# Performance work log

Hardware: AMD Instinct MI355X
Metric: run time of the kernel (lower is better)

## Reference

```python
import jax, jax.numpy as jnp
import numpy as np

N1 = 8000   # solute nodes
N2 = 8000   # solvent nodes
E = 128000  # edges per graph side (avg degree 16)
B = 128     # number of graphs in the batch
NFEAT, NHID, NCLS = 128, 256, 512
D = 2 * NCLS   # Set2Set input dim (1024)
H = D          # LSTM hidden = input_dim in DGL Set2Set


def setup_inputs() -> dict:
    key = jax.random.key(0)
    ks = jax.random.split(key, 24)
    w = lambda k, shp, fan: (jax.random.normal(k, shp, jnp.float32) / np.sqrt(fan))
    inp = {}
    inp["x1"] = jax.random.normal(ks[0], (N1, NFEAT), jnp.float32)
    inp["x2"] = jax.random.normal(ks[1], (N2, NFEAT), jnp.float32)
    inp["src1"] = jax.random.randint(ks[2], (E,), 0, N1, jnp.int32)
    inp["dst1"] = jax.random.randint(ks[3], (E,), 0, N1, jnp.int32)
    inp["src2"] = jax.random.randint(ks[4], (E,), 0, N2, jnp.int32)
    inp["dst2"] = jax.random.randint(ks[5], (E,), 0, N2, jnp.int32)
    inp["gid1"] = jnp.sort(jax.random.randint(ks[6], (N1,), 0, B, jnp.int32))
    inp["gid2"] = jnp.sort(jax.random.randint(ks[7], (N2,), 0, B, jnp.int32))
    # GraphConv weights (DGL stores W as [in, out]) + biases
    inp["W_gc1"] = w(ks[8], (NFEAT, NHID), NFEAT); inp["b_gc1"] = jnp.zeros((NHID,), jnp.float32)
    inp["W_gc2"] = w(ks[9], (NHID, NCLS), NHID);   inp["b_gc2"] = jnp.zeros((NCLS,), jnp.float32)
    inp["W_gc3"] = w(ks[10], (NFEAT, NHID), NFEAT); inp["b_gc3"] = jnp.zeros((NHID,), jnp.float32)
    inp["W_gc4"] = w(ks[11], (NHID, NCLS), NHID);   inp["b_gc4"] = jnp.zeros((NCLS,), jnp.float32)
    # Set2Set LSTM (input = 2*D, hidden = H), torch gate order i,f,g,o
    inp["W_ih"] = w(ks[12], (4 * H, 2 * D), 2 * D)
    inp["W_hh"] = w(ks[13], (4 * H, H), H)
    inp["b_ih"] = jnp.zeros((4 * H,), jnp.float32)
    inp["b_hh"] = jnp.zeros((4 * H,), jnp.float32)
    # MLP head
    inp["W_fc1"] = w(ks[14], (1024, 4096), 4096); inp["b_fc1"] = jnp.zeros((1024,), jnp.float32)
    inp["W_fc2"] = w(ks[15], (512, 1024), 1024);  inp["b_fc2"] = jnp.zeros((512,), jnp.float32)
    inp["W_fc3"] = w(ks[16], (1, 512), 512);      inp["b_fc3"] = jnp.zeros((1,), jnp.float32)
    return inp


def _gconv(x, src, dst, W, b, n):
    # DGL GraphConv, norm='both': D_out^{-1/2} scaling at src, sum over in-edges, D_in^{-1/2} at dst
    ones = jnp.ones(src.shape[0], x.dtype)
    outd = jnp.clip(jax.ops.segment_sum(ones, src, num_segments=n), 1.0)
    ind = jnp.clip(jax.ops.segment_sum(ones, dst, num_segments=n), 1.0)
    h = (x * (outd ** -0.5)[:, None]) @ W
    agg = jax.ops.segment_sum(h[src], dst, num_segments=n)   # sparse neighbor aggregation
    return agg * (ind ** -0.5)[:, None] + b


def _set2set(x, gid, Wih, Whh, bih, bhh):
    # DGL Set2Set, n_iters=2, 1-layer LSTM; x: [N, D], gid: [N] graph membership
    d = x.shape[1]
    q_star = jnp.zeros((B, 2 * d), x.dtype)
    h = jnp.zeros((B, d), x.dtype)
    c = jnp.zeros((B, d), x.dtype)
    for _ in range(2):
        gates = q_star @ Wih.T + h @ Whh.T + bih + bhh
        i, f, g, o = jnp.split(gates, 4, axis=1)
        c = jax.nn.sigmoid(f) * c + jax.nn.sigmoid(i) * jnp.tanh(g)
        h = jax.nn.sigmoid(o) * jnp.tanh(c)
        e = jnp.sum(x * h[gid], axis=1)                       # per-node attention logit
        m = jax.ops.segment_max(e, gid, num_segments=B)
        ex = jnp.exp(e - m[gid])
        s = jax.ops.segment_sum(ex, gid, num_segments=B)
        alpha = ex / s[gid]                                   # segment softmax
        r = jax.ops.segment_sum(alpha[:, None] * x, gid, num_segments=B)
        q_star = jnp.concatenate([h, r], axis=1)
    return q_star


def reference(x1, x2, src1, dst1, src2, dst2, gid1, gid2,
              W_gc1, b_gc1, W_gc2, b_gc2, W_gc3, b_gc3, W_gc4, b_gc4,
              W_ih, W_hh, b_ih, b_hh,
              W_fc1, b_fc1, W_fc2, b_fc2, W_fc3, b_fc3):
    s = jax.nn.relu(_gconv(x1, src1, dst1, W_gc1, b_gc1, N1))
    s = _gconv(s, src1, dst1, W_gc2, b_gc2, N1)
    v = jax.nn.relu(_gconv(x2, src2, dst2, W_gc3, b_gc3, N2))
    v = _gconv(v, src2, dst2, W_gc4, b_gc4, N2)
    # len_map = len1.T @ len2 == same-graph indicator for binary membership matrices
    len_map = (gid1[:, None] == gid2[None, :]).astype(s.dtype)
    imap = jnp.tanh(s @ v.T) * len_map                        # [N1, N2]
    solvent_prime = imap.T @ s                                # [N2, NCLS]
    solute_prime = imap @ v                                   # [N1, NCLS]
    sf = jnp.concatenate([s, solute_prime], axis=1)           # [N1, 2*NCLS]
    vf = jnp.concatenate([v, solvent_prime], axis=1)
    ss = _set2set(sf, gid1, W_ih, W_hh, b_ih, b_hh)           # [B, 4*NCLS]
    vs = _set2set(vf, gid2, W_ih, W_hh, b_ih, b_hh)
    z = jnp.concatenate([ss, vs], axis=1)                     # [B, 4096]
    z = jax.nn.relu(z @ W_fc1.T + b_fc1)
    z = jax.nn.relu(z @ W_fc2.T + b_fc2)
    return z @ W_fc3.T + b_fc3                                # [B, 1]
```

## Files before the change

kernel.cpp:

```cpp
#include <hip/hip_runtime.h>

#define DEV __device__ __forceinline__

typedef _Float16 half8 __attribute__((ext_vector_type(8)));
typedef _Float16 half4_t __attribute__((ext_vector_type(4)));
typedef float f32x4 __attribute__((ext_vector_type(4)));

DEV float ftanh(float x){
  float ax = fabsf(x);
  float e = __expf(-2.f*ax);
  float t = (1.f - e)/(1.f + e);
  return x < 0.f ? -t : t;
}
DEV float fsigm(float x){ return 1.f/(1.f + expf(-x)); }
DEV float wredsum(float v){
  #pragma unroll
  for (int o=32;o;o>>=1) v += __shfl_xor(v,o,64);
  return v;
}

__global__ void k_zero_i32(int* __restrict__ p, int n){
  int i = blockIdx.x*256 + threadIdx.x; if (i<n) p[i]=0;
}

__global__ void k_hist2(const int* __restrict__ s1, const int* __restrict__ d1, int E1,
                        int* __restrict__ co1, int* __restrict__ ci1,
                        const int* __restrict__ s2, const int* __restrict__ d2, int E2,
                        int* __restrict__ co2, int* __restrict__ ci2){
  int e = blockIdx.x*256 + threadIdx.x;
  if (e < E1){ atomicAdd(&co1[s1[e]],1); atomicAdd(&ci1[d1[e]],1); }
  int f = e - E1;
  if (f >= 0 && f < E2){ atomicAdd(&co2[s2[f]],1); atomicAdd(&ci2[d2[f]],1); }
}

__global__ void k_scan2(const int* __restrict__ c1, int n1, int* __restrict__ r1,
                        const int* __restrict__ c2, int n2, int* __restrict__ r2){
  __shared__ int sm[1024];
  const int* cnt = blockIdx.x ? c2 : c1;
  int*       row = blockIdx.x ? r2 : r1;
  int n          = blockIdx.x ? n2 : n1;
  int t = threadIdx.x;
  int per = n/1024 + 1;
  int st = t*per;
  int s = 0;
  for (int i=st;i<st+per;++i) if (i<n) s += cnt[i];
  sm[t]=s; __syncthreads();
  for (int o=1;o<1024;o<<=1){
    int v = (t>=o)? sm[t-o]:0;
    __syncthreads();
    sm[t] += v;
    __syncthreads();
  }
  int base = sm[t]-s;
  for (int i=st;i<st+per;++i){
    if (i<=n) row[i]=base;
    if (i<n) base += cnt[i];
  }
}

__global__ void k_scale2(const int* __restrict__ co1, const int* __restrict__ ci1, int n1,
                         float* __restrict__ os1, float* __restrict__ is1,
                         const int* __restrict__ co2, const int* __restrict__ ci2, int n2,
                         float* __restrict__ os2, float* __restrict__ is2){
  int i = blockIdx.x*256+threadIdx.x;
  if (i<n1){
    int a = co1[i] > 1 ? co1[i] : 1;
    int b = ci1[i] > 1 ? ci1[i] : 1;
    os1[i] = 1.f/sqrtf((float)a);
    is1[i] = 1.f/sqrtf((float)b);
  }
  int j = i - n1;
  if (j>=0 && j<n2){
    int a = co2[j] > 1 ? co2[j] : 1;
    int b = ci2[j] > 1 ? ci2[j] : 1;
    os2[j] = 1.f/sqrtf((float)a);
    is2[j] = 1.f/sqrtf((float)b);
  }
}

__global__ void k_scatter2(const int* __restrict__ s1, const int* __restrict__ d1, int E1,
                           const int* __restrict__ row1, int* __restrict__ cur1, int* __restrict__ csr1,
                           const int* __restrict__ s2, const int* __restrict__ d2, int E2,
                           const int* __restrict__ row2, int* __restrict__ cur2, int* __restrict__ csr2){
  int e = blockIdx.x*256+threadIdx.x;
  if (e<E1){ int d=d1[e]; int p=atomicAdd(&cur1[d],1); csr1[row1[d]+p]=s1[e]; }
  int f = e - E1;
  if (f>=0 && f<E2){ int d=d2[f]; int p=atomicAdd(&cur2[d],1); csr2[row2[d]+p]=s2[f]; }
}

__global__ void k_goff2(const int* __restrict__ g1, int n1, int* __restrict__ o1,
                        const int* __restrict__ g2, int n2, int* __restrict__ o2, int B){
  int t = threadIdx.x;
  const int* gid = (t>=256)? g2 : g1;
  int*      goff = (t>=256)? o2 : o1;
  int n          = (t>=256)? n2 : n1;
  int q = t & 255;
  if (q<=B){
    int lo=0, hi=n;
    while (lo<hi){ int mid=(lo+hi)>>1; if (gid[mid]<q) lo=mid+1; else hi=mid; }
    goff[q]=lo;
  }
}

__global__ void k_agg_h(const float* __restrict__ x, int ldx, const float* __restrict__ osc,
                        const int* __restrict__ row, const int* __restrict__ csr,
                        _Float16* __restrict__ oh, _Float16* __restrict__ ol, int n, int f4shift){
  int F4 = 1<<f4shift;
  int node = blockIdx.x*(256>>f4shift) + (threadIdx.x>>f4shift);
  if (node>=n) return;
  int fc = threadIdx.x & (F4-1);
  int F = F4<<2;
  int rs=row[node], re=row[node+1];
  float ax=0, ay=0, az=0, aw=0;
  if (osc){
    for (int e=rs;e<re;++e){
      int s = csr[e];
      float sc = osc[s];
      const float4 v = *(const float4*)(x + (size_t)s*ldx + (fc<<2));
      ax += sc*v.x; ay += sc*v.y; az += sc*v.z; aw += sc*v.w;
    }
  } else {
    int e = rs;
    for (; e+1<re; e+=2){
      int s0 = csr[e], s1 = csr[e+1];
      const float4 v0 = *(const float4*)(x + (size_t)s0*ldx + (fc<<2));
      const float4 v1 = *(const float4*)(x + (size_t)s1*ldx + (fc<<2));
      ax += v0.x+v1.x; ay += v0.y+v1.y; az += v0.z+v1.z; aw += v0.w+v1.w;
    }
    if (e<re){
      int s0 = csr[e];
      const float4 v0 = *(const float4*)(x + (size_t)s0*ldx + (fc<<2));
      ax += v0.x; ay += v0.y; az += v0.z; aw += v0.w;
    }
  }
  half4_t hv, lv;
  hv.x = (_Float16)ax; lv.x = (_Float16)(ax - (float)hv.x);
  hv.y = (_Float16)ay; lv.y = (_Float16)(ay - (float)hv.y);
  hv.z = (_Float16)az; lv.z = (_Float16)(az - (float)hv.z);
  hv.w = (_Float16)aw; lv.w = (_Float16)(aw - (float)hv.w);
  size_t o = (size_t)node*F + (fc<<2);
  *(half4_t*)(oh + o) = hv;
  *(half4_t*)(ol + o) = lv;
}

__global__ void k_wpack4(const float* __restrict__ W0, const float* __restrict__ W1,
                         const float* __restrict__ W2, const float* __restrict__ W3,
                         _Float16* __restrict__ h0, _Float16* __restrict__ l0,
                         _Float16* __restrict__ h1, _Float16* __restrict__ l1,
                         _Float16* __restrict__ h2, _Float16* __restrict__ l2,
                         _Float16* __restrict__ h3, _Float16* __restrict__ l3){
  int w = blockIdx.y;
  const float* W = (w==0)?W0:(w==1)?W1:(w==2)?W2:W3;
  _Float16* oh = (w==0)?h0:(w==1)?h1:(w==2)?h2:h3;
  _Float16* ol = (w==0)?l0:(w==1)?l1:(w==2)?l2:l3;
  int K   = (w&1)? 256 : 128;
  int nsh = (w&1)? 9 : 8;
  int i = blockIdx.x*256 + threadIdx.x;
  if (i >= (K<<nsh)) return;
  int k = i >> nsh, n = i & ((1<<nsh)-1);
  float v = W[i];
  _Float16 h = (_Float16)v;
  _Float16 l = (_Float16)(v - (float)h);
  size_t p = (((size_t)(k>>3)<<nsh) + n)*8 + (k&7);
  oh[p] = h; ol[p] = l;
}

__global__ __launch_bounds__(256)
void k_gconv_mfma(const _Float16* __restrict__ Ah0, const _Float16* __restrict__ Al0,
                  const _Float16* __restrict__ Ah1, const _Float16* __restrict__ Al1,
                  const _Float16* __restrict__ Bh0, const _Float16* __restrict__ Bl0,
                  const _Float16* __restrict__ Bh1, const _Float16* __restrict__ Bl1,
                  float* __restrict__ C0, float* __restrict__ C1, int ldc,
                  int M0, int M1, int N, int K,
                  const float* __restrict__ rs0, const float* __restrict__ rs1,
                  const float* __restrict__ bi0, const float* __restrict__ bi1, int relu,
                  const float* __restrict__ po0, const float* __restrict__ po1)
{
  __shared__ __align__(16) _Float16 As[2][4096];
  __shared__ __align__(16) _Float16 Bs[2][4096];

  const int gx = gridDim.x, gxy = gridDim.x*gridDim.y;
  const int nwg = gxy*2;
  int fid = blockIdx.x + gx*blockIdx.y + gxy*blockIdx.z;
  int q = nwg>>3, r = nwg&7;
  int xcd = fid & 7, idx = fid >> 3;
  int sid = (xcd<r ? xcd*(q+1) : r*(q+1)+(xcd-r)*q) + idx;
  const int z  = sid / gxy;  int rem = sid - z*gxy;
  const int by = rem / gx,  bx = rem - by*gx;

  const _Float16* Ah = z ? Ah1 : Ah0;
  const _Float16* Al = z ? Al1 : Al0;
  const _Float16* Bh = z ? Bh1 : Bh0;
  const _Float16* Bl = z ? Bl1 : Bl0;
  float*       C  = z ? C1 : C0;
  const float* rsc = z ? rs1 : rs0;
  const float* bia = z ? bi1 : bi0;
  const float* po  = z ? po1 : po0;
  const int M = z ? M1 : M0;

  const int row0 = by << 7;
  const int col0 = bx << 7;
  if (row0 >= ((M+127)&~127)) return;

  const int tid = threadIdx.x;
  const int am  = tid >> 2;
  const int akb = tid & 3;
  const int bn  = tid & 127;
  const int bkb = tid >> 7;
  const int wid = tid >> 6, lane = tid & 63;
  const int wr = wid >> 1, wc = wid & 1;
  const int lr = lane & 15, lg = lane >> 4;

  const size_t ldb8 = (size_t)N * 8;
  f32x4 acc[4][4] = {};

  const int kpt = K >> 5;
  const int nt  = 3 * kpt;

  half8 ga0, ga1, gb0, gb1;
  {
    const _Float16* Ap = Ah + (size_t)(row0 + am) * K + (akb<<3);
    ga0 = *(const half8*)(Ap);
    ga1 = *(const half8*)(Ap + (size_t)64 * K);
    const _Float16* Bp = Bh + (size_t)bkb * ldb8 + (size_t)(col0 + bn) * 8;
    gb0 = *(const half8*)(Bp);
    gb1 = *(const half8*)(Bp + 2*ldb8);
  }
  *(half8*)&As[0][(akb*128 + am)*8]        = ga0;
  *(half8*)&As[0][(akb*128 + am + 64)*8]   = ga1;
  *(half8*)&Bs[0][(bkb*128 + bn)*8]        = gb0;
  *(half8*)&Bs[0][((bkb+2)*128 + bn)*8]    = gb1;
  __syncthreads();

  int term = 0, kk = 32;
  if (kk == K){ kk = 0; term = 1; }
  for (int t = 0; t < nt; ++t){
    const int cb = t & 1;
    if (t + 1 < nt){
      const _Float16* Asrc = (term == 1) ? Al : Ah;
      const _Float16* Bsrc = (term == 2) ? Bl : Bh;
      const _Float16* Ap = Asrc + (size_t)(row0 + am) * K + kk + (akb<<3);
      ga0 = *(const half8*)(Ap);
      ga1 = *(const half8*)(Ap + (size_t)64 * K);
      const _Float16* Bp = Bsrc + (size_t)((kk>>3) + bkb) * ldb8 + (size_t)(col0 + bn) * 8;
      gb0 = *(const half8*)(Bp);
      gb1 = *(const half8*)(Bp + 2*ldb8);
      kk += 32; if (kk == K){ kk = 0; ++term; }
    }
    {
      const _Float16* Abase = &As[cb][((lg<<7) + (wr<<6) + lr)<<3];
      const _Float16* Bbase = &Bs[cb][((lg<<7) + (wc<<6) + lr)<<3];
      half8 af[4], bf[4];
      #pragma unroll
      for (int i=0;i<4;++i){
        af[i] = *(const half8*)(Abase + i*128);
        bf[i] = *(const half8*)(Bbase + i*128);
      }
      #pragma unroll
      for (int mi=0; mi<4; ++mi){
        #pragma unroll
        for (int ni=0; ni<4; ++ni){
          acc[mi][ni] = __builtin_amdgcn_mfma_f32_16x16x32_f16(af[mi], bf[ni], acc[mi][ni], 0, 0, 0);
        }
      }
    }
    if (t + 1 < nt){
      const int nb = cb ^ 1;
      *(half8*)&As[nb][(akb*128 + am)*8]      = ga0;
      *(half8*)&As[nb][(akb*128 + am + 64)*8] = ga1;
      *(half8*)&Bs[nb][(bkb*128 + bn)*8]      = gb0;
      *(half8*)&Bs[nb][((bkb+2)*128 + bn)*8]  = gb1;
    }
    __syncthreads();
  }

  #pragma unroll
  for (int ni = 0; ni < 4; ++ni){
    int cc = col0 + (wc<<6) + (ni<<4) + lr;
    float bv = bia ? bia[cc] : 0.f;
    #pragma unroll
    for (int mi = 0; mi < 4; ++mi){
      int rbase = row0 + (wr<<6) + (mi<<4) + (lg<<2);
      #pragma unroll
      for (int j = 0; j < 4; ++j){
        int rr = rbase + j;
        if (rr < M){
          float rs_ = rsc ? rsc[rr] : 1.f;
          float v = acc[mi][ni][j]*rs_ + bv;
          if (relu) v = fmaxf(v, 0.f);
          if (po) v *= po[rr];
          C[(size_t)rr*ldc + cc] = v;
        }
      }
    }
  }
}

__global__ __launch_bounds__(256)
void k_gemmsk(const float* __restrict__ Ab, size_t AsideOff, int lda,
              const float* __restrict__ Bm, int ldb,
              float* __restrict__ P, int M, int N, int kchunk)
{
  __shared__ float As[2][16][132];
  __shared__ float Bs[2][16][68];
  const int tid = threadIdx.x;
  const int col0 = (int)blockIdx.x << 6;
  const int kbeg = (int)blockIdx.z * kchunk;
  const float* A = Ab + (size_t)blockIdx.y * AsideOff;
  const int ar = tid >> 1, ak = (tid & 1) << 3;
  const int br = tid >> 2, bk = (tid & 3) << 2;
  const int tx = tid & 15, ty = tid >> 4;
  const float* Arow = A + (size_t)ar * lda + kbeg + ak;
  const float* Brow = Bm + (size_t)(col0 + br) * ldb + kbeg + bk;
  float acc[8][4] = {};
  float4 a0 = *(const float4*)(Arow);
  float4 a1 = *(const float4*)(Arow + 4);
  float4 b0 = *(const float4*)(Brow);
  As[0][ak+0][ar]=a0.x; As[0][ak+1][ar]=a0.y; As[0][ak+2][ar]=a0.z; As[0][ak+3][ar]=a0.w;
  As[0][ak+4][ar]=a1.x; As[0][ak+5][ar]=a1.y; As[0][ak+6][ar]=a1.z; As[0][ak+7][ar]=a1.w;
  Bs[0][bk+0][br]=b0.x; Bs[0][bk+1][br]=b0.y; Bs[0][bk+2][br]=b0.z; Bs[0][bk+3][br]=b0.w;
  __syncthreads();
  const int nt = kchunk >> 4;
  for (int t = 0; t < nt; ++t){
    const int cb = t & 1;
    if (t + 1 < nt){
      int k0 = (t + 1) << 4;
      a0 = *(const float4*)(Arow + k0);
      a1 = *(const float4*)(Arow + k0 + 4);
      b0 = *(const float4*)(Brow + k0);
    }
    #pragma unroll
    for (int kk = 0; kk < 16; ++kk){
      float4 b4 = *(const float4*)&Bs[cb][kk][tx << 2];
      float4 a4 = *(const float4*)&As[cb][kk][ty << 3];
      float4 a5 = *(const float4*)&As[cb][kk][(ty << 3) + 4];
      acc[0][0]+=a4.x*b4.x; acc[0][1]+=a4.x*b4.y; acc[0][2]+=a4.x*b4.z; acc[0][3]+=a4.x*b4.w;
      acc[1][0]+=a4.y*b4.x; acc[1][1]+=a4.y*b4.y; acc[1][2]+=a4.y*b4.z; acc[1][3]+=a4.y*b4.w;
      acc[2][0]+=a4.z*b4.x; acc[2][1]+=a4.z*b4.y; acc[2][2]+=a4.z*b4.z; acc[2][3]+=a4.z*b4.w;
      acc[3][0]+=a4.w*b4.x; acc[3][1]+=a4.w*b4.y; acc[3][2]+=a4.w*b4.z; acc[3][3]+=a4.w*b4.w;
      acc[4][0]+=a5.x*b4.x; acc[4][1]+=a5.x*b4.y; acc[4][2]+=a5.x*b4.z; acc[4][3]+=a5.x*b4.w;
      acc[5][0]+=a5.y*b4.x; acc[5][1]+=a5.y*b4.y; acc[5][2]+=a5.y*b4.z; acc[5][3]+=a5.y*b4.w;
      acc[6][0]+=a5.z*b4.x; acc[6][1]+=a5.z*b4.y; acc[6][2]+=a5.z*b4.z; acc[6][3]+=a5.z*b4.w;
      acc[7][0]+=a5.w*b4.x; acc[7][1]+=a5.w*b4.y; acc[7][2]+=a5.w*b4.z; acc[7][3]+=a5.w*b4.w;
    }
    if (t + 1 < nt){
      const int nb = cb ^ 1;
      As[nb][ak+0][ar]=a0.x; As[nb][ak+1][ar]=a0.y; As[nb][ak+2][ar]=a0.z; As[nb][ak+3][ar]=a0.w;
      As[nb][ak+4][ar]=a1.x; As[nb][ak+5][ar]=a1.y; As[nb][ak+6][ar]=a1.z; As[nb][ak+7][ar]=a1.w;
      Bs[nb][bk+0][br]=b0.x; Bs[nb][bk+1][br]=b0.y; Bs[nb][bk+2][br]=b0.z; Bs[nb][bk+3][br]=b0.w;
    }
    __syncthreads();
  }
  float* Pz = P + (size_t)(blockIdx.y*gridDim.z + blockIdx.z) * M * N;
  #pragma unroll
  for (int i = 0; i < 8; ++i){
    int rr = (ty << 3) + i;
    float4 v = {acc[i][0], acc[i][1], acc[i][2], acc[i][3]};
    *(float4*)(Pz + (size_t)rr*N + col0 + (tx<<2)) = v;
  }
}

__global__ void k_red_bias(const float* __restrict__ P, int split, int MN, int N,
                           const float* __restrict__ bias, float* __restrict__ C, int relu){
  int i = blockIdx.x*256 + threadIdx.x;
  if (i >= MN) return;
  float v = bias[i & (N-1)];
  for (int s=0;s<split;++s) v += P[(size_t)s*MN + i];
  if (relu) v = fmaxf(v, 0.f);
  C[i] = v;
}

__global__ __launch_bounds__(256)
void k_pairdot(const float* __restrict__ sf, const float* __restrict__ vf,
               const int* __restrict__ go1, const int* __restrict__ go2, float* __restrict__ T)
{
  __shared__ float As[16][68];
  __shared__ float Bs[16][68];
  int g = blockIdx.z;
  int it = blockIdx.y, jt = blockIdx.x;
  int gox = go1[g]; int cx = go1[g+1]-gox; if (cx>128) cx=128;
  int goy = go2[g]; int cy = go2[g+1]-goy; if (cy>128) cy=128;
  int cx64=(cx+63)&~63, cy64=(cy+63)&~63;
  int i0 = it<<6, j0 = jt<<6;
  if (i0 >= cx64 || j0 >= cy64) return;
  int tid=threadIdx.x, tx=tid&15, ty=tid>>4;
  int a_r = tid>>2, a_k=(tid&3)<<2;
  const float* Arow = sf + (size_t)(gox+i0+a_r)*1024;
  const float* Brow = vf + (size_t)(goy+j0+a_r)*1024;
  bool act = ((i0+(ty<<2)) < cx) && ((j0+(tx<<2)) < cy);
  float acc[4][4]={};
  for (int k0=0;k0<512;k0+=16){
    float4 av = *(const float4*)(Arow + k0 + a_k);
    float4 bv = *(const float4*)(Brow + k0 + a_k);
    As[a_k+0][a_r]=av.x; As[a_k+1][a_r]=av.y; As[a_k+2][a_r]=av.z; As[a_k+3][a_r]=av.w;
    Bs[a_k+0][a_r]=bv.x; Bs[a_k+1][a_r]=bv.y; Bs[a_k+2][a_r]=bv.z; Bs[a_k+3][a_r]=bv.w;
    __syncthreads();
    if (act){
      float4 a4 = *(const float4*)&As[0][ty<<2];
      float4 b4 = *(const float4*)&Bs[0][tx<<2];
      #pragma unroll
      for (int kk=0;kk<16;++kk){
        float4 na, nb;
        if (kk<15){
          na = *(const float4*)&As[kk+1][ty<<2];
          nb = *(const float4*)&Bs[kk+1][tx<<2];
        }
        acc[0][0] += a4.x*b4.x; acc[0][1] += a4.x*b4.y; acc[0][2] += a4.x*b4.z; acc[0][3] += a4.x*b4.w;
        acc[1][0] += a4.y*b4.x; acc[1][1] += a4.y*b4.y; acc[1][2] += a4.y*b4.z; acc[1][3] += a4.y*b4.w;
        acc[2][0] += a4.z*b4.x; acc[2][1] += a4.z*b4.y; acc[2][2] += a4.z*b4.z; acc[2][3] += a4.z*b4.w;
        acc[3][0] += a4.w*b4.x; acc[3][1] += a4.w*b4.y; acc[3][2] += a4.w*b4.z; acc[3][3] += a4.w*b4.w;
        if (kk<15){ a4 = na; b4 = nb; }
      }
    }
    __syncthreads();
  }
  float* Tg = T + (size_t)g*16384;
  #pragma unroll
  for (int ii=0; ii<4; ++ii){
    int gi = i0 + (ty<<2) + ii;
    int gj = j0 + (tx<<2);
    float4 v;
    v.x = (gi<cx && gj+0<cy) ? ftanh(acc[ii][0]) : 0.f;
    v.y = (gi<cx && gj+1<cy) ? ftanh(acc[ii][1]) : 0.f;
    v.z = (gi<cx && gj+2<cy) ? ftanh(acc[ii][2]) : 0.f;
    v.w = (gi<cx && gj+3<cy) ? ftanh(acc[ii][3]) : 0.f;
    *(float4*)(Tg + (size_t)gi*128 + gj) = v;
  }
}

template<bool TRANS>
__global__ __launch_bounds__(256)
void k_outapply(const float* __restrict__ T, const float* __restrict__ other,
                float* __restrict__ own, const int* __restrict__ goOwn, const int* __restrict__ goOther)
{
  __shared__ float As[16][68];
  __shared__ float Bs[16][68];
  int g = blockIdx.z;
  int r0 = (int)blockIdx.y<<6;
  int f0 = (int)blockIdx.x<<6;
  int gown = goOwn[g];   int cown = goOwn[g+1]-gown;   if (cown>128) cown=128;
  int goth = goOther[g]; int coth = goOther[g+1]-goth; if (coth>128) coth=128;
  int cr64 = (cown+63)&~63;
  if (r0 >= cr64) return;
  int K16 = (coth+15)&~15;
  const float* Tg = T + (size_t)g*16384;
  int tid=threadIdx.x, tx=tid&15, ty=tid>>4;
  bool act = (r0 + (ty<<2)) < cown;
  float acc[4][4]={};
  for (int ks=0; ks<K16; ks+=16){
    if (!TRANS){
      int rr = tid>>2, k4 = (tid&3)<<2;
      float4 av = *(const float4*)(Tg + (size_t)(r0+rr)*128 + ks + k4);
      As[k4+0][rr]=av.x; As[k4+1][rr]=av.y; As[k4+2][rr]=av.z; As[k4+3][rr]=av.w;
    } else {
      int kk = tid>>4, r4 = (tid&15)<<2;
      *(float4*)&As[kk][r4] = *(const float4*)(Tg + (size_t)(ks+kk)*128 + r0 + r4);
    }
    int bk = tid>>4, bf = (tid&15)<<2;
    *(float4*)&Bs[bk][bf] = *(const float4*)(other + (size_t)(goth+ks+bk)*1024 + f0 + bf);
    __syncthreads();
    if (act){
      float4 a4 = *(const float4*)&As[0][ty<<2];
      float4 b4 = *(const float4*)&Bs[0][tx<<2];
      #pragma unroll
      for (int kk=0;kk<16;++kk){
        float4 na, nb;
        if (kk<15){
          na = *(const float4*)&As[kk+1][ty<<2];
          nb = *(const float4*)&Bs[kk+1][tx<<2];
        }
        acc[0][0] += a4.x*b4.x; acc[0][1] += a4.x*b4.y; acc[0][2] += a4.x*b4.z; acc[0][3] += a4.x*b4.w;
        acc[1][0] += a4.y*b4.x; acc[1][1] += a4.y*b4.y; acc[1][2] += a4.y*b4.z; acc[1][3] += a4.y*b4.w;
        acc[2][0] += a4.z*b4.x; acc[2][1] += a4.z*b4.y; acc[2][2] += a4.z*b4.z; acc[2][3] += a4.z*b4.w;
        acc[3][0] += a4.w*b4.x; acc[3][1] += a4.w*b4.y; acc[3][2] += a4.w*b4.z; acc[3][3] += a4.w*b4.w;
        if (kk<15){ a4 = na; b4 = nb; }
      }
    }
    __syncthreads();
  }
  #pragma unroll
  for (int ii=0; ii<4; ++ii){
    int rr = r0 + (ty<<2) + ii;
    if (rr < cown){
      float4 v = {acc[ii][0],acc[ii][1],acc[ii][2],acc[ii][3]};
      *(float4*)(own + (size_t)(gown+rr)*1024 + 512 + f0 + (tx<<2)) = v;
    }
  }
}

__global__ void k_lstm1(const float* __restrict__ bih, const float* __restrict__ bhh,
                        float* __restrict__ c1, float* __restrict__ h1){
  int j = blockIdx.x*256 + threadIdx.x;
  if (j >= 1024) return;
  float gi = bih[j]        + bhh[j];
  float gg = bih[j+2048]   + bhh[j+2048];
  float go = bih[j+3072]   + bhh[j+3072];
  float cc = fsigm(gi)*ftanh(gg);
  c1[j] = cc;
  h1[j] = fsigm(go)*ftanh(cc);
}

__global__ void k_gemv_u(const float* __restrict__ Wih, const float* __restrict__ Whh,
                         const float* __restrict__ bih, const float* __restrict__ bhh,
                         const float* __restrict__ h1, float* __restrict__ u){
  int w = (blockIdx.x*256 + threadIdx.x)>>6;
  int lane = threadIdx.x & 63;
  if (w >= 4096) return;
  const float* wi = Wih + (size_t)w*2048;
  const float* wh = Whh + (size_t)w*1024;
  float acc = 0.f;
  #pragma unroll
  for (int qq=0;qq<4;++qq){
    int o = qq*256 + (lane<<2);
    float4 hv = *(const float4*)(h1 + o);
    float4 a  = *(const float4*)(wi + o);
    float4 b  = *(const float4*)(wh + o);
    acc += hv.x*(a.x+b.x) + hv.y*(a.y+b.y) + hv.z*(a.z+b.z) + hv.w*(a.w+b.w);
  }
  acc = wredsum(acc);
  if (lane==0) u[w] = acc + bih[w] + bhh[w];
}

__global__ __launch_bounds__(256)
void k_attn(const float* __restrict__ sf, const float* __restrict__ vf,
            const int* __restrict__ go1, const int* __restrict__ go2,
            const float* __restrict__ hbase, size_t hSideOff, int hstride,
            float* __restrict__ outbase, size_t oSideOff, int ldout)
{
  __shared__ float hs[1024];
  __shared__ float ech[1024];
  __shared__ float red[8];
  int side = blockIdx.y;
  const float* x = side? vf : sf;
  const int* goff = side? go2 : go1;
  const float* hsrc = hbase + (size_t)side*hSideOff;
  float* outp = outbase + (size_t)side*oSideOff;
  int b = blockIdx.x, t = threadIdx.x;
  int i0 = goff[b], i1 = goff[b+1];
  int lane = t & 63, wv = t >> 6;
  { float4 hv = *(const float4*)(hsrc + (size_t)b*hstride + (t<<2));
    *(float4*)&hs[t<<2] = hv; }
  __syncthreads();
  float m = -3.0e38f, s = 0.f;
  float ax=0, ay=0, az=0, aw=0;
  for (int c = i0; c < i1; c += 1024){
    int ce = c + 1024; if (ce > i1) ce = i1;
    int n = ce - c;
    float wmax = -3.0e38f;
    for (int i = c + wv; i < ce; i += 4){
      const float* xr = x + (size_t)i*1024;
      float d = 0.f;
      #pragma unroll
      for (int qq=0;qq<4;++qq){
        int o = qq*256 + (lane<<2);
        float4 xv = *(const float4*)(xr+o);
        float4 h4 = *(const float4*)&hs[o];
        d += xv.x*h4.x + xv.y*h4.y + xv.z*h4.z + xv.w*h4.w;
      }
      d = wredsum(d);
      if (lane==0) ech[i-c] = d;
      wmax = fmaxf(wmax, d);
    }
    if (lane==0) red[wv] = wmax;
    __syncthreads();
    float cm = fmaxf(fmaxf(red[0],red[1]), fmaxf(red[2],red[3]));
    float nm = fmaxf(m, cm);
    float scale = __expf(m - nm);
    s *= scale; ax*=scale; ay*=scale; az*=scale; aw*=scale;
    float ps = 0.f;
    for (int k = t; k < n; k += 256) ps += __expf(ech[k]-nm);
    ps = wredsum(ps);
    __syncthreads();
    if (lane==0) red[wv] = ps;
    __syncthreads();
    s += red[0]+red[1]+red[2]+red[3];
    for (int k = 0; k < n; ++k){
      float w = __expf(ech[k]-nm);
      float4 xv = *(const float4*)(x + (size_t)(c+k)*1024 + (t<<2));
      ax += w*xv.x; ay += w*xv.y; az += w*xv.z; aw += w*xv.w;
    }
    m = nm;
    __syncthreads();
  }
  float inv = (i1>i0 && s>0.f) ? 1.f/s : 0.f;
  float4 o = {ax*inv, ay*inv, az*inv, aw*inv};
  *(float4*)(outp + (size_t)b*ldout + (t<<2)) = o;
}

__global__ void k_lstm2_red(const float* __restrict__ Pb, size_t PsideOff, int split,
                            const float* __restrict__ u, const float* __restrict__ c1,
                            float* __restrict__ z, int B){
  int idx = blockIdx.x*256 + threadIdx.x;
  if (idx >= B*1024) return;
  int side = blockIdx.y;
  const float* P = Pb + (size_t)side*PsideOff;
  int b = idx >> 10, j = idx & 1023;
  float gi=u[j], gf=u[j+1024], gg=u[j+2048], go=u[j+3072];
  const float* g = P + (size_t)b*4096;
  for (int s=0;s<split;++s){
    const float* gs = g + (size_t)s*B*4096;
    gi += gs[j]; gf += gs[j+1024]; gg += gs[j+2048]; go += gs[j+3072];
  }
  float cc = fsigm(gf)*c1[j] + fsigm(gi)*ftanh(gg);
  z[(size_t)b*4096 + side*2048 + j] = fsigm(go)*ftanh(cc);
}

__global__ void k_fc3(const float* __restrict__ z2, const float* __restrict__ w3,
                      const float* __restrict__ b3, float* __restrict__ out, int B){
  int wv = (blockIdx.x*256+threadIdx.x)>>6;
  int lane = threadIdx.x & 63;
  if (wv >= B) return;
  const float* zr = z2 + (size_t)wv*512;
  float acc=0.f;
  #pragma unroll
  for (int qq=0;qq<2;++qq){
    int o = qq*256 + (lane<<2);
    float4 a  = *(const float4*)(zr + o);
    float4 ww = *(const float4*)(w3 + o);
    acc += a.x*ww.x + a.y*ww.y + a.z*ww.z + a.w*ww.w;
  }
  acc = wredsum(acc);
  if (lane==0) out[wv] = acc + b3[0];
}

extern "C" void kernel_launch(void* const* d_in, const int* in_sizes, int n_in,
                              void* d_out, int out_size, void* d_ws, size_t ws_size,
                              hipStream_t stream)
{
  const float* x1  = (const float*)d_in[0];
  const float* x2  = (const float*)d_in[1];
  const int* src1  = (const int*)d_in[2];
  const int* dst1  = (const int*)d_in[3];
  const int* src2  = (const int*)d_in[4];
  const int* dst2  = (const int*)d_in[5];
  const int* gid1  = (const int*)d_in[6];
  const int* gid2  = (const int*)d_in[7];
  const float* Wg1 = (const float*)d_in[8];  const float* bg1 = (const float*)d_in[9];
  const float* Wg2 = (const float*)d_in[10]; const float* bg2 = (const float*)d_in[11];
  const float* Wg3 = (const float*)d_in[12]; const float* bg3 = (const float*)d_in[13];
  const float* Wg4 = (const float*)d_in[14]; const float* bg4 = (const float*)d_in[15];
  const float* Wih = (const float*)d_in[16]; const float* Whh = (const float*)d_in[17];
  const float* bih = (const float*)d_in[18]; const float* bhh = (const float*)d_in[19];
  const float* Wf1 = (const float*)d_in[20]; const float* bf1 = (const float*)d_in[21];
  const float* Wf2 = (const float*)d_in[22]; const float* bf2 = (const float*)d_in[23];
  const float* Wf3 = (const float*)d_in[24]; const float* bf3 = (const float*)d_in[25];
  float* out = (float*)d_out;

  const int N1 = in_sizes[0]/128;
  const int N2 = in_sizes[1]/128;
  const int E1 = in_sizes[2];
  const int E2 = in_sizes[4];
  const int B  = out_size;
  const int NM = N1>N2?N1:N2;

  char* base = (char*)d_ws; size_t off=0;
  auto alloc = [&](size_t bytes)->void*{ void* p = base+off; off += (bytes+255)&~(size_t)255; return p; };

  int* zr   = (int*)alloc(sizeof(int)*(size_t)(3*N1+3*N2));
  int* co1=zr, *ci1=zr+N1, *cur1=zr+2*N1;
  int* co2=zr+3*N1, *ci2=zr+3*N1+N2, *cur2=zr+3*N1+2*N2;
  int* row1 = (int*)alloc(sizeof(int)*(size_t)(N1+1));
  int* row2 = (int*)alloc(sizeof(int)*(size_t)(N2+1));
  int* csr1 = (int*)alloc(sizeof(int)*(size_t)E1);
  int* csr2 = (int*)alloc(sizeof(int)*(size_t)E2);
  int* go1  = (int*)alloc(sizeof(int)*(size_t)(B+1));
  int* go2  = (int*)alloc(sizeof(int)*(size_t)(B+1));
  float* os1 = (float*)alloc(sizeof(float)*(size_t)N1);
  float* is1 = (float*)alloc(sizeof(float)*(size_t)N1);
  float* os2 = (float*)alloc(sizeof(float)*(size_t)N2);
  float* is2 = (float*)alloc(sizeof(float)*(size_t)N2);
  _Float16* a1h = (_Float16*)alloc(sizeof(_Float16)*(size_t)(NM+128)*256);
  _Float16* a1l = (_Float16*)alloc(sizeof(_Float16)*(size_t)(NM+128)*256);
  _Float16* a2h = (_Float16*)alloc(sizeof(_Float16)*(size_t)(NM+128)*256);
  _Float16* a2l = (_Float16*)alloc(sizeof(_Float16)*(size_t)(NM+128)*256);
  _Float16* wg1h = (_Float16*)alloc(sizeof(_Float16)*32768);
  _Float16* wg1l = (_Float16*)alloc(sizeof(_Float16)*32768);
  _Float16* wg2h = (_Float16*)alloc(sizeof(_Float16)*131072);
  _Float16* wg2l = (_Float16*)alloc(sizeof(_Float16)*131072);
  _Float16* wg3h = (_Float16*)alloc(sizeof(_Float16)*32768);
  _Float16* wg3l = (_Float16*)alloc(sizeof(_Float16)*32768);
  _Float16* wg4h = (_Float16*)alloc(sizeof(_Float16)*131072);
  _Float16* wg4l = (_Float16*)alloc(sizeof(_Float16)*131072);
  float* sf  = (float*)alloc(sizeof(float)*(size_t)(N1+128)*1024);
  float* vf  = (float*)alloc(sizeof(float)*(size_t)(N2+128)*1024);
  float* h1 = (float*)alloc(sizeof(float)*1024);
  float* c1 = (float*)alloc(sizeof(float)*1024);
  float* u  = (float*)alloc(sizeof(float)*4096);
  float* r1 = (float*)alloc(sizeof(float)*(size_t)2*B*1024);
  float* z1 = (float*)alloc(sizeof(float)*(size_t)B*1024);
  float* z2 = (float*)alloc(sizeof(float)*(size_t)B*512);
  float* z  = (float*)alloc(sizeof(float)*(size_t)B*4096);
  float* T  = (float*)alloc(sizeof(float)*(size_t)B*16384);
  float* Pbuf = (float*)alloc(sizeof(float)*(size_t)16*B*1024*4);
  if (off > ws_size) return;

  float* hb1 = sf + 512;
  float* hb2 = vf + 512;

  dim3 blk(256);

  k_wpack4<<<dim3(512,4),blk,0,stream>>>(Wg1,Wg2,Wg3,Wg4,
                                         wg1h,wg1l, wg2h,wg2l, wg3h,wg3l, wg4h,wg4l);

  k_zero_i32<<<(3*N1+3*N2+255)/256, blk, 0, stream>>>(zr, 3*N1+3*N2);
  k_hist2<<<(E1+E2+255)/256, blk, 0, stream>>>(src1,dst1,E1,co1,ci1, src2,dst2,E2,co2,ci2);
  k_scan2<<<2,1024,0,stream>>>(ci1,N1,row1, ci2,N2,row2);
  k_scale2<<<(N1+N2+255)/256,blk,0,stream>>>(co1,ci1,N1,os1,is1, co2,ci2,N2,os2,is2);
  k_scatter2<<<(E1+E2+255)/256,blk,0,stream>>>(src1,dst1,E1,row1,cur1,csr1, src2,dst2,E2,row2,cur2,csr2);
  k_goff2<<<1,512,0,stream>>>(gid1,N1,go1, gid2,N2,go2, B);

  int gy = (NM+127)/128;
  k_agg_h<<<(N1+7)/8,blk,0,stream>>>(x1,128, os1,row1,csr1, a1h,a1l, N1,5);
  k_agg_h<<<(N2+7)/8,blk,0,stream>>>(x2,128, os2,row2,csr2, a2h,a2l, N2,5);
  k_gconv_mfma<<<dim3(2,gy,2),blk,0,stream>>>(a1h,a1l, a2h,a2l,
                                              wg1h,wg1l, wg3h,wg3l,
                                              hb1,hb2,1024, N1,N2, 256,128,
                                              is1,is2, bg1,bg3, 1, os1,os2);
  k_agg_h<<<(N1+3)/4,blk,0,stream>>>(hb1,1024, nullptr,row1,csr1, a1h,a1l, N1,6);
  k_agg_h<<<(N2+3)/4,blk,0,stream>>>(hb2,1024, nullptr,row2,csr2, a2h,a2l, N2,6);
  k_gconv_mfma<<<dim3(4,gy,2),blk,0,stream>>>(a1h,a1l, a2h,a2l,
                                              wg2h,wg2l, wg4h,wg4l,
                                              sf,vf,1024, N1,N2, 512,256,
                                              is1,is2, bg2,bg4, 0, nullptr,nullptr);

  k_pairdot<<<dim3(2,2,B),blk,0,stream>>>(sf,vf,go1,go2,T);
  k_outapply<false><<<dim3(8,2,B),blk,0,stream>>>(T,vf,sf,go1,go2);
  k_outapply<true ><<<dim3(8,2,B),blk,0,stream>>>(T,sf,vf,go2,go1);

  k_lstm1<<<4,blk,0,stream>>>(bih,bhh,c1,h1);
  k_gemv_u<<<1024,blk,0,stream>>>(Wih,Whh,bih,bhh,h1,u);

  k_attn<<<dim3(B,2),blk,0,stream>>>(sf,vf,go1,go2, h1,0,0, r1,(size_t)B*1024,1024);
  k_gemmsk<<<dim3(64,2,4),blk,0,stream>>>(r1,(size_t)B*1024,1024, Wih+1024,2048, Pbuf, 128,4096,256);
  k_lstm2_red<<<dim3((B*1024+255)/256,2),blk,0,stream>>>(Pbuf,(size_t)4*B*4096,4, u,c1, z,B);
  k_attn<<<dim3(B,2),blk,0,stream>>>(sf,vf,go1,go2, z,2048,4096, z+1024,2048,4096);

  k_gemmsk<<<dim3(16,1,16),blk,0,stream>>>(z,0,4096, Wf1,4096, Pbuf, 128,1024,256);
  k_red_bias<<<(B*1024+255)/256,blk,0,stream>>>(Pbuf,16,B*1024,1024,bf1,z1,1);
  k_gemmsk<<<dim3(8,1,8),blk,0,stream>>>(z1,0,1024, Wf2,1024, Pbuf, 128,512,128);
  k_red_bias<<<(B*512+255)/256,blk,0,stream>>>(Pbuf,8,B*512,512,bf2,z2,1);
  k_fc3<<<(B*64+255)/256,blk,0,stream>>>(z2,Wf3,bf3,out,B);
}
```

Before: 415.4 us.

## Replace FP32 interaction kernels with fused split-FP16 MFMA pack+interact kernels

Removes the scalar-FP32 pairdot and two outapply kernels and replaces them with a pack kernel plus one fused interact kernel. The pack kernel converts per-graph, 32-row padded blocks of s/v into hi/lo FP16 pairs. The interact kernel computes tanh(s·vᵀ) with 3-term split-FP16 MFMA, keeps the tanh matrix in LDS instead of a global T buffer, and applies it to the other side's packed features with MFMA. The packed buffers share memory with Pbuf. The aim is to move the work onto matrix cores and drop the global round-trip of T, at the cost of pack overhead, three times the MFMA count, and only 2*B blocks of parallelism.

```diff
diff --git a/kernel.cpp b/kernel.cpp
--- a/kernel.cpp
+++ b/kernel.cpp
@@ -17,6 +17,18 @@
   #pragma unroll
   for (int o=32;o;o>>=1) v += __shfl_xor(v,o,64);
   return v;
+}
+DEV f32x4 MF(half8 a, half8 b, f32x4 c){
+  return __builtin_amdgcn_mfma_f32_16x16x32_f16(a,b,c,0,0,0);
+}
+DEV void split8(float4 a0, float4 a1, half8& h, half8& l){
+  float f[8] = {a0.x,a0.y,a0.z,a0.w,a1.x,a1.y,a1.z,a1.w};
+  #pragma unroll
+  for (int e=0;e<8;++e){
+    _Float16 hh = (_Float16)f[e];
+    h[e] = hh;
+    l[e] = (_Float16)(f[e] - (float)hh);
+  }
 }
 
 __global__ void k_zero_i32(int* __restrict__ p, int n){
@@ -89,7 +101,9 @@
 }
 
 __global__ void k_goff2(const int* __restrict__ g1, int n1, int* __restrict__ o1,
-                        const int* __restrict__ g2, int n2, int* __restrict__ o2, int B){
+                        const int* __restrict__ g2, int n2, int* __restrict__ o2, int B,
+                        int* __restrict__ pb1, int* __restrict__ gm1,
+                        int* __restrict__ pb2, int* __restrict__ gm2){
   int t = threadIdx.x;
   const int* gid = (t>=256)? g2 : g1;
   int*      goff = (t>=256)? o2 : o1;
@@ -99,6 +113,22 @@
     int lo=0, hi=n;
     while (lo<hi){ int mid=(lo+hi)>>1; if (gid[mid]<q) lo=mid+1; else hi=mid; }
     goff[q]=lo;
+  }
+  __syncthreads();
+  if (t==0 || t==256){
+    const int* go = t ? o2 : o1;
+    int* pb = t ? pb2 : pb1;
+    int* gm = t ? gm2 : gm1;
+    int acc = 0;
+    for (int g=0; g<B; ++g){
+      pb[g] = acc;
+      int c = go[g+1]-go[g]; if (c>128) c=128;
+      int pc = (c+31)&~31;
+      int nb = pc>>5;
+      for (int k=0;k<nb;++k) gm[(acc>>5)+k] = g;
+      acc += pc;
+    }
+    pb[B] = acc;
   }
 }
 
@@ -265,11 +295,11 @@
       }
     }
     if (t + 1 < nt){
-      const int nb = cb ^ 1;
-      *(half8*)&As[nb][(akb*128 + am)*8]      = ga0;
-      *(half8*)&As[nb][(akb*128 + am + 64)*8] = ga1;
-      *(half8*)&Bs[nb][(bkb*128 + bn)*8]      = gb0;
-      *(half8*)&Bs[nb][((bkb+2)*128 + bn)*8]  = gb1;
+      const int nb_ = cb ^ 1;
+      *(half8*)&As[nb_][(akb*128 + am)*8]      = ga0;
+      *(half8*)&As[nb_][(akb*128 + am + 64)*8] = ga1;
+      *(half8*)&Bs[nb_][(bkb*128 + bn)*8]      = gb0;
+      *(half8*)&Bs[nb_][((bkb+2)*128 + bn)*8]  = gb1;
     }
     __syncthreads();
   }
@@ -290,6 +320,189 @@
           if (relu) v = fmaxf(v, 0.f);
           if (po) v *= po[rr];
           C[(size_t)rr*ldc + cc] = v;
+        }
+      }
+    }
+  }
+}
+
+__global__ __launch_bounds__(256)
+void k_pack(const float* __restrict__ sf, const float* __restrict__ vf,
+            const int* __restrict__ go1, const int* __restrict__ go2,
+            const int* __restrict__ pb1, const int* __restrict__ pb2,
+            const int* __restrict__ gm1, const int* __restrict__ gm2,
+            _Float16* __restrict__ p1h, _Float16* __restrict__ p1l,
+            _Float16* __restrict__ p2h, _Float16* __restrict__ p2l, int B)
+{
+  __shared__ float st[32][516];
+  const int side = blockIdx.y;
+  const float* x = side ? vf : sf;
+  const int* go = side ? go2 : go1;
+  const int* pb = side ? pb2 : pb1;
+  const int* gm = side ? gm2 : gm1;
+  _Float16* ph = side ? p2h : p1h;
+  _Float16* pl = side ? p2l : p1l;
+  const int u = blockIdx.x;
+  if (u*32 >= pb[B]) return;
+  const int g = gm[u];
+  const int j0 = u*32 - pb[g];
+  const int base = go[g];
+  int cnt = go[g+1]-base; if (cnt>128) cnt=128;
+  const int t = threadIdx.x;
+  const int r = t>>3, f0 = (t&7)<<2;
+  const bool valid = (j0 + r) < cnt;
+  const float* src = x + (size_t)(base + j0 + r)*1024;
+  #pragma unroll
+  for (int q=0;q<16;++q){
+    int f = f0 + (q<<5);
+    float4 vv;
+    if (valid) vv = *(const float4*)(src + f);
+    else { vv.x=0.f; vv.y=0.f; vv.z=0.f; vv.w=0.f; }
+    *(float4*)&st[r][f] = vv;
+  }
+  __syncthreads();
+  #pragma unroll
+  for (int q=0;q<8;++q){
+    int u2 = t + (q<<8);
+    int jg = u2>>9, f = u2&511;
+    half8 h8, l8;
+    #pragma unroll
+    for (int e=0;e<8;++e){
+      float vvv = st[(jg<<3)+e][f];
+      _Float16 hh = (_Float16)vvv;
+      h8[e]=hh; l8[e]=(_Float16)(vvv-(float)hh);
+    }
+    size_t a = ((size_t)((u<<2)+jg)<<12) + ((size_t)f<<3);
+    *(half8*)(ph + a) = h8;
+    *(half8*)(pl + a) = l8;
+  }
+}
+
+template<int NS, int NTT>
+DEV void phase1(const float* __restrict__ own, const float* __restrict__ oth,
+                int gR, int gO, int cR, int cO, int w, int lr, int lg,
+                _Float16* __restrict__ Th, _Float16* __restrict__ Tl)
+{
+  f32x4 acc[NS][NTT];
+  #pragma unroll
+  for (int s=0;s<NS;++s)
+    #pragma unroll
+    for (int c=0;c<NTT;++c) acc[s][c] = (f32x4){0.f,0.f,0.f,0.f};
+  for (int k0=0;k0<512;k0+=32){
+    half8 bh[NTT], bl[NTT];
+    #pragma unroll
+    for (int cj=0;cj<NTT;++cj){
+      const float* Brow = oth + (size_t)(gO + (cj<<4) + lr)*1024 + k0 + (lg<<3);
+      split8(*(const float4*)(Brow), *(const float4*)(Brow+4), bh[cj], bl[cj]);
+    }
+    #pragma unroll
+    for (int s=0;s<NS;++s){
+      const float* Arow = own + (size_t)(gR + ((w+s*4)<<4) + lr)*1024 + k0 + (lg<<3);
+      half8 ah, al;
+      split8(*(const float4*)(Arow), *(const float4*)(Arow+4), ah, al);
+      #pragma unroll
+      for (int cj=0;cj<NTT;++cj){
+        acc[s][cj] = MF(ah, bh[cj], acc[s][cj]);
+        acc[s][cj] = MF(al, bh[cj], acc[s][cj]);
+        acc[s][cj] = MF(ah, bl[cj], acc[s][cj]);
+      }
+    }
+  }
+  #pragma unroll
+  for (int s=0;s<NS;++s){
+    int rbase = ((w+s*4)<<4) + (lg<<2);
+    #pragma unroll
+    for (int cj=0;cj<NTT;++cj){
+      int c = (cj<<4) + lr;
+      #pragma unroll
+      for (int qq=0;qq<4;++qq){
+        int r = rbase + qq;
+        float t = (r<cR && c<cO) ? ftanh(acc[s][cj][qq]) : 0.f;
+        _Float16 hh = (_Float16)t;
+        Th[r*136 + c] = hh;
+        Tl[r*136 + c] = (_Float16)(t - (float)hh);
+      }
+    }
+  }
+}
+
+__global__ __launch_bounds__(256)
+void k_interact(const float* __restrict__ sf, const float* __restrict__ vf,
+                const int* __restrict__ go1, const int* __restrict__ go2,
+                const int* __restrict__ pb1, const int* __restrict__ pb2,
+                const _Float16* __restrict__ p1h, const _Float16* __restrict__ p1l,
+                const _Float16* __restrict__ p2h, const _Float16* __restrict__ p2l,
+                float* __restrict__ sfo, float* __restrict__ vfo)
+{
+  __shared__ __align__(16) _Float16 Th[128*136];
+  __shared__ __align__(16) _Float16 Tl[128*136];
+  const int side = blockIdx.x, g = blockIdx.y;
+  const float* own = side ? vf : sf;
+  const float* oth = side ? sf : vf;
+  const _Float16* oph = side ? p1h : p2h;
+  const _Float16* opl = side ? p1l : p2l;
+  const int* goR = side ? go2 : go1;
+  const int* goO = side ? go1 : go2;
+  const int* pbO = side ? pb1 : pb2;
+  float* outp = side ? vfo : sfo;
+  int gR = goR[g]; int cR = goR[g+1]-gR; if (cR>128) cR=128;
+  int gO = goO[g]; int cO = goO[g+1]-gO; if (cO>128) cO=128;
+  const int pO = pbO[g];
+  const int cO32 = (cO+31)&~31;
+  const int cR64 = (cR+63)&~63;
+  const int tid = threadIdx.x, w = tid>>6, lane = tid&63;
+  const int lr = lane&15, lg = lane>>4;
+  const int MR = cR64>>4;
+  const int wideN = (cO32 > 64);
+  if (MR == 4){
+    if (!wideN) phase1<1,4>(own,oth,gR,gO,cR,cO,w,lr,lg,Th,Tl);
+    else        phase1<1,8>(own,oth,gR,gO,cR,cO,w,lr,lg,Th,Tl);
+  } else if (MR == 8){
+    if (!wideN) phase1<2,4>(own,oth,gR,gO,cR,cO,w,lr,lg,Th,Tl);
+    else        phase1<2,8>(own,oth,gR,gO,cR,cO,w,lr,lg,Th,Tl);
+  }
+  __syncthreads();
+  const int RT = MR, ks = cO32>>5;
+  for (int rc=0; rc<RT; rc+=4){
+    #pragma unroll
+    for (int fc=0; fc<2; ++fc){
+      const int ft0 = (w<<3) + (fc<<2);
+      f32x4 acc[4][4];
+      #pragma unroll
+      for (int a_=0;a_<4;++a_)
+        #pragma unroll
+        for (int b_=0;b_<4;++b_) acc[a_][b_] = (f32x4){0.f,0.f,0.f,0.f};
+      for (int k=0;k<ks;++k){
+        half8 tbh[4], tbl[4];
+        #pragma unroll
+        for (int rt=0;rt<4;++rt){
+          int a = (((rc+rt)<<4) + lr)*136 + (k<<5) + (lg<<3);
+          tbh[rt] = *(const half8*)&Th[a];
+          tbl[rt] = *(const half8*)&Tl[a];
+        }
+        const size_t kb = ((size_t)(pO>>3) + (k<<2) + lg)<<12;
+        #pragma unroll
+        for (int ft=0; ft<4; ++ft){
+          size_t a = kb + ((size_t)(((ft0+ft)<<4) + lr) << 3);
+          half8 pah = *(const half8*)(oph + a);
+          half8 pal = *(const half8*)(opl + a);
+          #pragma unroll
+          for (int rt=0;rt<4;++rt){
+            acc[ft][rt] = MF(pah, tbh[rt], acc[ft][rt]);
+            acc[ft][rt] = MF(pal, tbh[rt], acc[ft][rt]);
+            acc[ft][rt] = MF(pah, tbl[rt], acc[ft][rt]);
+          }
+        }
+      }
+      #pragma unroll
+      for (int ft=0; ft<4; ++ft){
+        #pragma unroll
+        for (int rt=0;rt<4;++rt){
+          int r = ((rc+rt)<<4) + lr;
+          if (r < cR){
+            float4 vv = {acc[ft][rt][0],acc[ft][rt][1],acc[ft][rt][2],acc[ft][rt][3]};
+            *(float4*)(outp + (size_t)(gR + r)*1024 + 512 + ((ft0+ft)<<4) + (lg<<2)) = vv;
+          }
         }
       }
     }
@@ -368,124 +581,6 @@
   for (int s=0;s<split;++s) v += P[(size_t)s*MN + i];
   if (relu) v = fmaxf(v, 0.f);
   C[i] = v;
-}
-
-__global__ __launch_bounds__(256)
-void k_pairdot(const float* __restrict__ sf, const float* __restrict__ vf,
-               const int* __restrict__ go1, const int* __restrict__ go2, float* __restrict__ T)
-{
-  __shared__ float As[16][68];
-  __shared__ float Bs[16][68];
-  int g = blockIdx.z;
-  int it = blockIdx.y, jt = blockIdx.x;
-  int gox = go1[g]; int cx = go1[g+1]-gox; if (cx>128) cx=128;
-  int goy = go2[g]; int cy = go2[g+1]-goy; if (cy>128) cy=128;
-  int cx64=(cx+63)&~63, cy64=(cy+63)&~63;
-  int i0 = it<<6, j0 = jt<<6;
-  if (i0 >= cx64 || j0 >= cy64) return;
-  int tid=threadIdx.x, tx=tid&15, ty=tid>>4;
-  int a_r = tid>>2, a_k=(tid&3)<<2;
-  const float* Arow = sf + (size_t)(gox+i0+a_r)*1024;
-  const float* Brow = vf + (size_t)(goy+j0+a_r)*1024;
-  bool act = ((i0+(ty<<2)) < cx) && ((j0+(tx<<2)) < cy);
-  float acc[4][4]={};
-  for (int k0=0;k0<512;k0+=16){
-    float4 av = *(const float4*)(Arow + k0 + a_k);
-    float4 bv = *(const float4*)(Brow + k0 + a_k);
-    As[a_k+0][a_r]=av.x; As[a_k+1][a_r]=av.y; As[a_k+2][a_r]=av.z; As[a_k+3][a_r]=av.w;
-    Bs[a_k+0][a_r]=bv.x; Bs[a_k+1][a_r]=bv.y; Bs[a_k+2][a_r]=bv.z; Bs[a_k+3][a_r]=bv.w;
-    __syncthreads();
-    if (act){
-      float4 a4 = *(const float4*)&As[0][ty<<2];
-      float4 b4 = *(const float4*)&Bs[0][tx<<2];
-      #pragma unroll
-      for (int kk=0;kk<16;++kk){
-        float4 na, nb;
-        if (kk<15){
-          na = *(const float4*)&As[kk+1][ty<<2];
-          nb = *(const float4*)&Bs[kk+1][tx<<2];
-        }
-        acc[0][0] += a4.x*b4.x; acc[0][1] += a4.x*b4.y; acc[0][2] += a4.x*b4.z; acc[0][3] += a4.x*b4.w;
-        acc[1][0] += a4.y*b4.x; acc[1][1] += a4.y*b4.y; acc[1][2] += a4.y*b4.z; acc[1][3] += a4.y*b4.w;
-        acc[2][0] += a4.z*b4.x; acc[2][1] += a4.z*b4.y; acc[2][2] += a4.z*b4.z; acc[2][3] += a4.z*b4.w;
-        acc[3][0] += a4.w*b4.x; acc[3][1] += a4.w*b4.y; acc[3][2] += a4.w*b4.z; acc[3][3] += a4.w*b4.w;
-        if (kk<15){ a4 = na; b4 = nb; }
-      }
-    }
-    __syncthreads();
-  }
-  float* Tg = T + (size_t)g*16384;
-  #pragma unroll
-  for (int ii=0; ii<4; ++ii){
-    int gi = i0 + (ty<<2) + ii;
-    int gj = j0 + (tx<<2);
-    float4 v;
-    v.x = (gi<cx && gj+0<cy) ? ftanh(acc[ii][0]) : 0.f;
-    v.y = (gi<cx && gj+1<cy) ? ftanh(acc[ii][1]) : 0.f;
-    v.z = (gi<cx && gj+2<cy) ? ftanh(acc[ii][2]) : 0.f;
-    v.w = (gi<cx && gj+3<cy) ? ftanh(acc[ii][3]) : 0.f;
-    *(float4*)(Tg + (size_t)gi*128 + gj) = v;
-  }
-}
-
-template<bool TRANS>
-__global__ __launch_bounds__(256)
-void k_outapply(const float* __restrict__ T, const float* __restrict__ other,
-                float* __restrict__ own, const int* __restrict__ goOwn, const int* __restrict__ goOther)
-{
-  __shared__ float As[16][68];
-  __shared__ float Bs[16][68];
-  int g = blockIdx.z;
-  int r0 = (int)blockIdx.y<<6;
-  int f0 = (int)blockIdx.x<<6;
-  int gown = goOwn[g];   int cown = goOwn[g+1]-gown;   if (cown>128) cown=128;
-  int goth = goOther[g]; int coth = goOther[g+1]-goth; if (coth>128) coth=128;
-  int cr64 = (cown+63)&~63;
-  if (r0 >= cr64) return;
-  int K16 = (coth+15)&~15;
-  const float* Tg = T + (size_t)g*16384;
-  int tid=threadIdx.x, tx=tid&15, ty=tid>>4;
-  bool act = (r0 + (ty<<2)) < cown;
-  float acc[4][4]={};
-  for (int ks=0; ks<K16; ks+=16){
-    if (!TRANS){
-      int rr = tid>>2, k4 = (tid&3)<<2;
-      float4 av = *(const float4*)(Tg + (size_t)(r0+rr)*128 + ks + k4);
-      As[k4+0][rr]=av.x; As[k4+1][rr]=av.y; As[k4+2][rr]=av.z; As[k4+3][rr]=av.w;
-    } else {
-      int kk = tid>>4, r4 = (tid&15)<<2;
-      *(float4*)&As[kk][r4] = *(const float4*)(Tg + (size_t)(ks+kk)*128 + r0 + r4);
-    }
-    int bk = tid>>4, bf = (tid&15)<<2;
-    *(float4*)&Bs[bk][bf] = *(const float4*)(other + (size_t)(goth+ks+bk)*1024 + f0 + bf);
-    __syncthreads();
-    if (act){
-      float4 a4 = *(const float4*)&As[0][ty<<2];
-      float4 b4 = *(const float4*)&Bs[0][tx<<2];
-      #pragma unroll
-      for (int kk=0;kk<16;++kk){
-        float4 na, nb;
-        if (kk<15){
-          na = *(const float4*)&As[kk+1][ty<<2];
-          nb = *(const float4*)&Bs[kk+1][tx<<2];
-        }
-        acc[0][0] += a4.x*b4.x; acc[0][1] += a4.x*b4.y; acc[0][2] += a4.x*b4.z; acc[0][3] += a4.x*b4.w;
-        acc[1][0] += a4.y*b4.x; acc[1][1] += a4.y*b4.y; acc[1][2] += a4.y*b4.z; acc[1][3] += a4.y*b4.w;
-        acc[2][0] += a4.z*b4.x; acc[2][1] += a4.z*b4.y; acc[2][2] += a4.z*b4.z; acc[2][3] += a4.z*b4.w;
-        acc[3][0] += a4.w*b4.x; acc[3][1] += a4.w*b4.y; acc[3][2] += a4.w*b4.z; acc[3][3] += a4.w*b4.w;
-        if (kk<15){ a4 = na; b4 = nb; }
-      }
-    }
-    __syncthreads();
-  }
-  #pragma unroll
-  for (int ii=0; ii<4; ++ii){
-    int rr = r0 + (ty<<2) + ii;
-    if (rr < cown){
-      float4 v = {acc[ii][0],acc[ii][1],acc[ii][2],acc[ii][3]};
-      *(float4*)(own + (size_t)(gown+rr)*1024 + 512 + f0 + (tx<<2)) = v;
-    }
-  }
 }
 
 __global__ void k_lstm1(const float* __restrict__ bih, const float* __restrict__ bhh,
@@ -665,6 +760,10 @@
   int* csr2 = (int*)alloc(sizeof(int)*(size_t)E2);
   int* go1  = (int*)alloc(sizeof(int)*(size_t)(B+1));
   int* go2  = (int*)alloc(sizeof(int)*(size_t)(B+1));
+  int* pb1  = (int*)alloc(sizeof(int)*(size_t)(B+1));
+  int* pb2  = (int*)alloc(sizeof(int)*(size_t)(B+1));
+  int* gm1  = (int*)alloc(sizeof(int)*1024);
+  int* gm2  = (int*)alloc(sizeof(int)*1024);
   float* os1 = (float*)alloc(sizeof(float)*(size_t)N1);
   float* is1 = (float*)alloc(sizeof(float)*(size_t)N1);
   float* os2 = (float*)alloc(sizeof(float)*(size_t)N2);
@@ -690,8 +789,16 @@
   float* z1 = (float*)alloc(sizeof(float)*(size_t)B*1024);
   float* z2 = (float*)alloc(sizeof(float)*(size_t)B*512);
   float* z  = (float*)alloc(sizeof(float)*(size_t)B*4096);
-  float* T  = (float*)alloc(sizeof(float)*(size_t)B*16384);
-  float* Pbuf = (float*)alloc(sizeof(float)*(size_t)16*B*1024*4);
+  const int PN = ((NM + 32*B + 63)&~63) + 64;
+  const size_t PE = (size_t)PN*512;
+  size_t packedBytes = 4*PE*sizeof(_Float16);
+  size_t pbufBytes   = sizeof(float)*(size_t)16*B*1024*4;
+  char* uni = (char*)alloc(packedBytes > pbufBytes ? packedBytes : pbufBytes);
+  _Float16* p1h = (_Float16*)uni;
+  _Float16* p1l = p1h + PE;
+  _Float16* p2h = p1l + PE;
+  _Float16* p2l = p2h + PE;
+  float* Pbuf = (float*)uni;
   if (off > ws_size) return;
 
   float* hb1 = sf + 512;
@@ -707,7 +814,7 @@
   k_scan2<<<2,1024,0,stream>>>(ci1,N1,row1, ci2,N2,row2);
   k_scale2<<<(N1+N2+255)/256,blk,0,stream>>>(co1,ci1,N1,os1,is1, co2,ci2,N2,os2,is2);
   k_scatter2<<<(E1+E2+255)/256,blk,0,stream>>>(src1,dst1,E1,row1,cur1,csr1, src2,dst2,E2,row2,cur2,csr2);
-  k_goff2<<<1,512,0,stream>>>(gid1,N1,go1, gid2,N2,go2, B);
+  k_goff2<<<1,512,0,stream>>>(gid1,N1,go1, gid2,N2,go2, B, pb1,gm1, pb2,gm2);
 
   int gy = (NM+127)/128;
   k_agg_h<<<(N1+7)/8,blk,0,stream>>>(x1,128, os1,row1,csr1, a1h,a1l, N1,5);
@@ -723,9 +830,11 @@
                                               sf,vf,1024, N1,N2, 512,256,
                                               is1,is2, bg2,bg4, 0, nullptr,nullptr);
 
-  k_pairdot<<<dim3(2,2,B),blk,0,stream>>>(sf,vf,go1,go2,T);
-  k_outapply<false><<<dim3(8,2,B),blk,0,stream>>>(T,vf,sf,go1,go2);
-  k_outapply<true ><<<dim3(8,2,B),blk,0,stream>>>(T,sf,vf,go2,go1);
+  const int GMAX = NM/32 + B + 2;
+  k_pack<<<dim3(GMAX,2),blk,0,stream>>>(sf,vf, go1,go2, pb1,pb2, gm1,gm2,
+                                        p1h,p1l, p2h,p2l, B);
+  k_interact<<<dim3(2,B),blk,0,stream>>>(sf,vf, go1,go2, pb1,pb2,
+                                         p1h,p1l, p2h,p2l, sf,vf);
 
   k_lstm1<<<4,blk,0,stream>>>(bih,bhh,c1,h1);
   k_gemv_u<<<1024,blk,0,stream>>>(Wih,Whh,bih,bhh,h1,u);
```

Result: slower. 461.4 us (+11.1%).
